# Optimization experiments

Hardware: AMD Instinct MI355X
Metric: run time of the kernel (lower is better)

The kernel has to match this reference:

```python
import jax, jax.numpy as jnp
import numpy as np
import math

SEQLEN, DIM, N_HEADS = 2048, 4096, 32
HEAD_DIM = DIM // N_HEADS
NEG_INF = -1e30  # exp underflows to exactly 0, same effect as -inf without NaN risk


def setup_inputs() -> dict:
    key = jax.random.key(0)
    ks = jax.random.split(key, 7)
    scale = 1.0 / math.sqrt(DIM)
    x = jax.random.normal(ks[0], (SEQLEN, DIM), dtype=jnp.float32)
    weight_q = jax.random.normal(ks[1], (DIM, DIM), dtype=jnp.float32) * scale
    weight_k = jax.random.normal(ks[2], (DIM, DIM), dtype=jnp.float32) * scale
    weight_v = jax.random.normal(ks[3], (DIM, DIM), dtype=jnp.float32) * scale
    weight_o = jax.random.normal(ks[4], (DIM, DIM), dtype=jnp.float32) * scale
    # RoPE frequencies: freqs_cis = exp(i * t * theta_j), standard LLaMA schedule
    inv_freq = 1.0 / (10000.0 ** (np.arange(0, HEAD_DIM, 2, dtype=np.float32) / HEAD_DIM))
    angles = np.arange(SEQLEN, dtype=np.float32)[:, None] * inv_freq[None, :]  # [S, hd/2]
    freqs_cos = jnp.asarray(np.cos(angles), dtype=jnp.float32)
    freqs_sin = jnp.asarray(np.sin(angles), dtype=jnp.float32)
    # additive causal mask [S, S]
    mask = jnp.where(jnp.triu(jnp.ones((SEQLEN, SEQLEN), dtype=bool), k=1), NEG_INF, 0.0).astype(jnp.float32)
    return {"x": x, "weight_q": weight_q, "weight_k": weight_k, "weight_v": weight_v,
            "weight_o": weight_o, "freqs_cos": freqs_cos, "freqs_sin": freqs_sin,
            "mask": mask, "start_pos": 0}


def _apply_rope(t, cos, sin):
    # t: [S, H, hd]; cos/sin: [S, hd/2]
    tr = t.reshape(*t.shape[:-1], -1, 2)           # [S, H, hd/2, 2]
    t_re, t_im = tr[..., 0], tr[..., 1]
    c = cos[:, None, :]
    s = sin[:, None, :]
    out_re = t_re * c - t_im * s
    out_im = t_re * s + t_im * c
    return jnp.stack([out_re, out_im], axis=-1).reshape(t.shape)


def reference(x, weight_q, weight_k, weight_v, weight_o, freqs_cos, freqs_sin, mask, start_pos):
    S, D = x.shape
    hd = freqs_cos.shape[-1] * 2
    H = D // hd
    # the per-head double loop over wq[j][i] is exactly a full [D,D] projection
    xq = (x @ weight_q).reshape(S, H, hd)
    xk = (x @ weight_k).reshape(S, H, hd)
    xv = (x @ weight_v).reshape(S, H, hd)
    xq = _apply_rope(xq, freqs_cos, freqs_sin)
    xk = _apply_rope(xk, freqs_cos, freqs_sin)
    # start_pos == 0 prefill: cache slice == freshly computed keys/values
    scores = jnp.einsum('shd,thd->hst', xq, xk) / jnp.sqrt(jnp.float32(hd))
    scores = scores + mask[None, :, :]
    probs = jax.nn.softmax(scores.astype(jnp.float32), axis=-1).astype(xq.dtype)
    qkv = jnp.einsum('hst,thd->shd', probs, xv).reshape(S, D)
    return qkv @ weight_o
```

## Files before the change

### kernel.cpp

```cpp
#include <hip/hip_runtime.h>
#include <hip/hip_bf16.h>
#include <type_traits>

typedef __hip_bfloat16 bf16;
typedef __attribute__((ext_vector_type(8))) short s8v;
typedef __attribute__((ext_vector_type(4))) short s4v;
typedef __attribute__((ext_vector_type(4))) float f4v;

#define MFMA16(A, B, C) __builtin_amdgcn_mfma_f32_16x16x32_bf16((A), (B), (C), 0, 0, 0)

constexpr int SEQ = 2048;
constexpr int DIM = 4096;
constexpr int NH  = 32;
constexpr int HD  = 128;

__device__ __forceinline__ short f2bs(float f) {
    __hip_bfloat16_raw r = __float2bfloat16(f);
    return (short)r.x;
}

__device__ __forceinline__ void ld_g2l(const bf16* g, bf16* l) {
    __builtin_amdgcn_global_load_lds(
        (const __attribute__((address_space(1))) void*)g,
        (__attribute__((address_space(3))) void*)l, 16, 0, 0);
}

__global__ void convert_bf16(const float* __restrict__ s, bf16* __restrict__ d) {
    int i = blockIdx.x * blockDim.x + threadIdx.x;
    float4 f = ((const float4*)s)[i];
    s4v o;
    o[0] = f2bs(f.x); o[1] = f2bs(f.y); o[2] = f2bs(f.z); o[3] = f2bs(f.w);
    *(s4v*)(d + (size_t)i * 4) = o;
}

__global__ void convt_bf16(const float* __restrict__ src, bf16* __restrict__ dst,
                           int R, int C) {
    __shared__ float t[32][33];
    int c0 = blockIdx.x * 32, r0 = blockIdx.y * 32;
    int tx = threadIdx.x, ty = threadIdx.y;
#pragma unroll
    for (int i = 0; i < 4; i++)
        t[ty + 8 * i][tx] = src[(size_t)(r0 + ty + 8 * i) * C + c0 + tx];
    __syncthreads();
#pragma unroll
    for (int i = 0; i < 4; i++)
        dst[(size_t)(c0 + ty + 8 * i) * R + r0 + tx] = __float2bfloat16(t[tx][ty + 8 * i]);
}

template <typename CT>
__global__ __launch_bounds__(256) void gemm_lds(const bf16* __restrict__ A,
                                                const bf16* __restrict__ Bt,
                                                CT* __restrict__ C,
                                                int M, int N, int K) {
    __shared__ bf16 As[128 * 32];
    __shared__ bf16 Bs[128 * 32];
    const int tid  = threadIdx.x;
    const int lane = tid & 63;
    const int w    = tid >> 6;
    const int m16  = lane & 15;
    const int quad = lane >> 4;
    const int wm   = w >> 1, wn = w & 1;
    const int bm   = blockIdx.y, bn = blockIdx.x;

    const bf16* Ab = A  + (size_t)bm * 128 * K;
    const bf16* Bb = Bt + (size_t)bn * 128 * K;

    const int lrow = lane >> 2;
    const int lcol = (lane & 3) * 8;

    f4v acc[4][4] = {};

    for (int k0 = 0; k0 < K; k0 += 32) {
#pragma unroll
        for (int rep = 0; rep < 2; rep++) {
            int c = w * 2 + rep;
            ld_g2l(Ab + (size_t)(c * 16 + lrow) * K + k0 + lcol, As + c * 512);
            ld_g2l(Bb + (size_t)(c * 16 + lrow) * K + k0 + lcol, Bs + c * 512);
        }
        __syncthreads();

        s8v a[4], b[4];
#pragma unroll
        for (int i = 0; i < 4; i++)
            a[i] = *(s8v*)(As + (wm * 64 + i * 16 + m16) * 32 + quad * 8);
#pragma unroll
        for (int j = 0; j < 4; j++)
            b[j] = *(s8v*)(Bs + (wn * 64 + j * 16 + m16) * 32 + quad * 8);
#pragma unroll
        for (int i = 0; i < 4; i++)
#pragma unroll
            for (int j = 0; j < 4; j++) acc[i][j] = MFMA16(a[i], b[j], acc[i][j]);
        __syncthreads();
    }

#pragma unroll
    for (int i = 0; i < 4; i++)
#pragma unroll
        for (int j = 0; j < 4; j++)
#pragma unroll
            for (int r = 0; r < 4; r++) {
                int row = bm * 128 + wm * 64 + i * 16 + quad * 4 + r;
                int col = bn * 128 + wn * 64 + j * 16 + m16;
                if constexpr (std::is_same<CT, float>::value)
                    C[(size_t)row * N + col] = acc[i][j][r];
                else
                    C[(size_t)row * N + col] = __float2bfloat16(acc[i][j][r]);
            }
}

template <typename AT, typename CT>
__global__ __launch_bounds__(256) void gemm_nat(const AT* __restrict__ A,
                                                const float* __restrict__ B,
                                                CT* __restrict__ C,
                                                int M, int N, int K) {
    __shared__ short As[128][40];
    __shared__ short Bs[128][40];
    const int tid  = threadIdx.x;
    const int lane = tid & 63;
    const int w    = tid >> 6;
    const int m16  = lane & 15;
    const int quad = lane >> 4;
    const int wm   = w >> 1, wn = w & 1;
    const int bm   = blockIdx.y, bn = blockIdx.x;

    const AT* Ab = A + (size_t)bm * 128 * K;

    f4v acc[4][4] = {};
    const int r0 = tid >> 2;
    const int kc = (tid & 3) * 8;

    for (int k0 = 0; k0 < K; k0 += 32) {
        if constexpr (std::is_same<AT, float>::value) {
#pragma unroll
            for (int half = 0; half < 2; half++) {
                const float* src = Ab + (size_t)(r0 + 64 * half) * K + k0 + kc;
                float4 f0 = *(const float4*)(src);
                float4 f1 = *(const float4*)(src + 4);
                s8v t;
                t[0] = f2bs(f0.x); t[1] = f2bs(f0.y); t[2] = f2bs(f0.z); t[3] = f2bs(f0.w);
                t[4] = f2bs(f1.x); t[5] = f2bs(f1.y); t[6] = f2bs(f1.z); t[7] = f2bs(f1.w);
                *(s8v*)&As[r0 + 64 * half][kc] = t;
            }
        } else {
            *(s8v*)&As[r0][kc]      = *(const s8v*)(Ab + (size_t)r0 * K + k0 + kc);
            *(s8v*)&As[r0 + 64][kc] = *(const s8v*)(Ab + (size_t)(r0 + 64) * K + k0 + kc);
        }
#pragma unroll
        for (int v = tid; v < 512; v += 256) {
            int kr = v >> 4;
            int nc = (v & 15) * 8;
            const float* src = B + (size_t)(k0 + kr) * N + bn * 128 + nc;
            float4 f0 = *(const float4*)(src);
            float4 f1 = *(const float4*)(src + 4);
            Bs[nc + 0][kr] = f2bs(f0.x); Bs[nc + 1][kr] = f2bs(f0.y);
            Bs[nc + 2][kr] = f2bs(f0.z); Bs[nc + 3][kr] = f2bs(f0.w);
            Bs[nc + 4][kr] = f2bs(f1.x); Bs[nc + 5][kr] = f2bs(f1.y);
            Bs[nc + 6][kr] = f2bs(f1.z); Bs[nc + 7][kr] = f2bs(f1.w);
        }
        __syncthreads();

        s8v a[4], b[4];
#pragma unroll
        for (int i = 0; i < 4; i++) a[i] = *(s8v*)&As[wm * 64 + i * 16 + m16][quad * 8];
#pragma unroll
        for (int j = 0; j < 4; j++) b[j] = *(s8v*)&Bs[wn * 64 + j * 16 + m16][quad * 8];
#pragma unroll
        for (int i = 0; i < 4; i++)
#pragma unroll
            for (int j = 0; j < 4; j++) acc[i][j] = MFMA16(a[i], b[j], acc[i][j]);
        __syncthreads();
    }

#pragma unroll
    for (int i = 0; i < 4; i++)
#pragma unroll
        for (int j = 0; j < 4; j++)
#pragma unroll
            for (int r = 0; r < 4; r++) {
                int row = bm * 128 + wm * 64 + i * 16 + quad * 4 + r;
                int col = bn * 128 + wn * 64 + j * 16 + m16;
                if constexpr (std::is_same<CT, float>::value)
                    C[(size_t)row * N + col] = acc[i][j][r];
                else
                    C[(size_t)row * N + col] = __float2bfloat16(acc[i][j][r]);
            }
}

__global__ void rope_kernel(bf16* __restrict__ Q, bf16* __restrict__ K,
                            const float* __restrict__ fc, const float* __restrict__ fs) {
    int tid = blockIdx.x * blockDim.x + threadIdx.x;
    int s = tid >> 11;
    int r = tid & 2047;
    int i = r & 63;
    float c  = fc[s * 64 + i];
    float sn = fs[s * 64 + i];
    size_t idx = (size_t)s * DIM + 2 * r;
    float qre = __bfloat162float(Q[idx]), qim = __bfloat162float(Q[idx + 1]);
    Q[idx]     = __float2bfloat16(qre * c - qim * sn);
    Q[idx + 1] = __float2bfloat16(qre * sn + qim * c);
    float kre = __bfloat162float(K[idx]), kim = __bfloat162float(K[idx + 1]);
    K[idx]     = __float2bfloat16(kre * c - kim * sn);
    K[idx + 1] = __float2bfloat16(kre * sn + kim * c);
}

__global__ __launch_bounds__(256) void attn_kernel(const bf16* __restrict__ Q,
                                                   const bf16* __restrict__ K,
                                                   const bf16* __restrict__ V,
                                                   bf16* __restrict__ O) {
    __shared__ short Ks[64][136];
    __shared__ short Vs[128][72];
    __shared__ short Ps[64][72];

    const int qb = (int)gridDim.x - 1 - (int)blockIdx.x;
    const int h  = blockIdx.y;
    const int tid  = threadIdx.x;
    const int w    = tid >> 6;
    const int lane = tid & 63;
    const int m16  = lane & 15;
    const int quad = lane >> 4;
    const float scale = 0.08838834764831845f;

    const int rn  = tid >> 4;
    const int rc  = (tid & 15) * 8;
    const int dcs = (tid & 15) & 7;

    s8v aq[4];
    {
        const bf16* qp = Q + (size_t)(qb * 64 + w * 16 + m16) * DIM + h * HD + quad * 8;
#pragma unroll
        for (int ks = 0; ks < 4; ks++) aq[ks] = *(const s8v*)(qp + ks * 32);
    }

    f4v acc[8] = {};
    float mrow[4] = {-1e30f, -1e30f, -1e30f, -1e30f};
    float lrow[4] = {};

    s8v kreg[4], vreg[4];
    {
        const bf16* kp = K + (size_t)rn * DIM + h * HD + rc;
        const bf16* vp = V + (size_t)rn * DIM + h * HD + rc;
#pragma unroll
        for (int it = 0; it < 4; it++) {
            kreg[it] = *(const s8v*)(kp + (size_t)it * 16 * DIM);
            vreg[it] = *(const s8v*)(vp + (size_t)it * 16 * DIM);
        }
    }

    for (int kt = 0; kt <= qb; kt++) {
#pragma unroll
        for (int it = 0; it < 4; it++)
            *(s8v*)&Ks[it * 16 + rn][rc] = kreg[it];
#pragma unroll
        for (int it = 0; it < 4; it++) {
            int n   = it * 16 + rn;
            int col = (((n >> 3) ^ dcs) << 3) | (n & 7);
#pragma unroll
            for (int e = 0; e < 8; e++) Vs[rc + e][col] = vreg[it][e];
        }
        __syncthreads();

        if (kt < qb) {
            const bf16* kp = K + (size_t)((kt + 1) * 64 + rn) * DIM + h * HD + rc;
            const bf16* vp = V + (size_t)((kt + 1) * 64 + rn) * DIM + h * HD + rc;
#pragma unroll
            for (int it = 0; it < 4; it++) {
                kreg[it] = *(const s8v*)(kp + (size_t)it * 16 * DIM);
                vreg[it] = *(const s8v*)(vp + (size_t)it * 16 * DIM);
            }
        }

        f4v sc[4] = {};
#pragma unroll
        for (int j = 0; j < 4; j++)
#pragma unroll
            for (int ks = 0; ks < 4; ks++) {
                s8v bk = *(s8v*)&Ks[j * 16 + m16][ks * 32 + quad * 8];
                sc[j] = MFMA16(aq[ks], bk, sc[j]);
            }

        const bool diag = (kt == qb);
#pragma unroll
        for (int j = 0; j < 4; j++)
#pragma unroll
            for (int r = 0; r < 4; r++) {
                float sv = sc[j][r] * scale;
                if (diag && (j * 16 + m16) > (w * 16 + quad * 4 + r)) sv = -1e30f;
                sc[j][r] = sv;
            }

#pragma unroll
        for (int r = 0; r < 4; r++) {
            float mx = fmaxf(fmaxf(sc[0][r], sc[1][r]), fmaxf(sc[2][r], sc[3][r]));
#pragma unroll
            for (int off = 1; off < 16; off <<= 1) mx = fmaxf(mx, __shfl_xor(mx, off, 64));
            float mn    = fmaxf(mrow[r], mx);
            float alpha = __expf(mrow[r] - mn);
            mrow[r] = mn;
            float rs = 0.f;
#pragma unroll
            for (int j = 0; j < 4; j++) {
                float p = __expf(sc[j][r] - mn);
                sc[j][r] = p;
                rs += p;
            }
#pragma unroll
            for (int off = 1; off < 16; off <<= 1) rs += __shfl_xor(rs, off, 64);
            lrow[r] = lrow[r] * alpha + rs;
#pragma unroll
            for (int jo = 0; jo < 8; jo++) acc[jo][r] = acc[jo][r] * alpha;
        }

#pragma unroll
        for (int j = 0; j < 4; j++)
#pragma unroll
            for (int r = 0; r < 4; r++)
                Ps[w * 16 + quad * 4 + r][j * 16 + m16] = f2bs(sc[j][r]);
        asm volatile("s_waitcnt lgkmcnt(0)" ::: "memory");
        __builtin_amdgcn_sched_barrier(0);

#pragma unroll
        for (int ks2 = 0; ks2 < 2; ks2++) {
            s8v ap = *(s8v*)&Ps[w * 16 + m16][ks2 * 32 + quad * 8];
#pragma unroll
            for (int jo = 0; jo < 8; jo++) {
                int dv = jo * 16 + m16;
                int cg = (((ks2 * 4 + quad) ^ ((dv >> 3) & 7)) << 3);
                s8v bv = *(s8v*)&Vs[dv][cg];
                acc[jo] = MFMA16(ap, bv, acc[jo]);
            }
        }
        __syncthreads();
    }

#pragma unroll
    for (int jo = 0; jo < 8; jo++)
#pragma unroll
        for (int r = 0; r < 4; r++) {
            float o = acc[jo][r] / fmaxf(lrow[r], 1e-30f);
            int row = qb * 64 + w * 16 + quad * 4 + r;
            int col = h * HD + jo * 16 + m16;
            O[(size_t)row * DIM + col] = __float2bfloat16(o);
        }
}

extern "C" void kernel_launch(void* const* d_in, const int* in_sizes, int n_in,
                              void* d_out, int out_size, void* d_ws, size_t ws_size,
                              hipStream_t stream) {
    const float* x  = (const float*)d_in[0];
    const float* wq = (const float*)d_in[1];
    const float* wk = (const float*)d_in[2];
    const float* wv = (const float*)d_in[3];
    const float* wo = (const float*)d_in[4];
    const float* fc = (const float*)d_in[5];
    const float* fs = (const float*)d_in[6];

    float* out = (float*)d_out;

    const size_t SZ = (size_t)SEQ * DIM;
    const size_t WZ = (size_t)DIM * DIM;
    bf16* Q  = (bf16*)d_ws;
    bf16* Kb = Q + SZ;
    bf16* V  = Kb + SZ;
    bf16* AO = V + SZ;

    dim3 gG(DIM / 128, SEQ / 128);
    const size_t need = (5 * SZ + WZ) * sizeof(bf16);

    if (ws_size >= need) {
        bf16* xb = AO + SZ;
        bf16* wb = xb + SZ;

        dim3 tB(32, 8), tGw(DIM / 32, DIM / 32);

        convert_bf16<<<(int)(SZ / 4 / 256), 256, 0, stream>>>(x, xb);

        convt_bf16<<<tGw, tB, 0, stream>>>(wq, wb, DIM, DIM);
        gemm_lds<bf16><<<gG, 256, 0, stream>>>(xb, wb, Q, SEQ, DIM, DIM);
        convt_bf16<<<tGw, tB, 0, stream>>>(wk, wb, DIM, DIM);
        gemm_lds<bf16><<<gG, 256, 0, stream>>>(xb, wb, Kb, SEQ, DIM, DIM);
        convt_bf16<<<tGw, tB, 0, stream>>>(wv, wb, DIM, DIM);
        gemm_lds<bf16><<<gG, 256, 0, stream>>>(xb, wb, V, SEQ, DIM, DIM);

        rope_kernel<<<(SEQ * (DIM / 2)) / 256, 256, 0, stream>>>(Q, Kb, fc, fs);
        attn_kernel<<<dim3(SEQ / 64, NH), 256, 0, stream>>>(Q, Kb, V, AO);

        convt_bf16<<<tGw, tB, 0, stream>>>(wo, wb, DIM, DIM);
        gemm_lds<float><<<gG, 256, 0, stream>>>(AO, wb, out, SEQ, DIM, DIM);
    } else {
        gemm_nat<float, bf16><<<gG, 256, 0, stream>>>(x, wq, Q,  SEQ, DIM, DIM);
        gemm_nat<float, bf16><<<gG, 256, 0, stream>>>(x, wk, Kb, SEQ, DIM, DIM);
        gemm_nat<float, bf16><<<gG, 256, 0, stream>>>(x, wv, V,  SEQ, DIM, DIM);
        rope_kernel<<<(SEQ * (DIM / 2)) / 256, 256, 0, stream>>>(Q, Kb, fc, fs);
        attn_kernel<<<dim3(SEQ / 64, NH), 256, 0, stream>>>(Q, Kb, V, AO);
        gemm_nat<bf16, float><<<gG, 256, 0, stream>>>(AO, wo, out, SEQ, DIM, DIM);
    }
}
```

Measured before the change: 916.8 us.

## Replace projection GEMM with double-buffered 8-wave 128x256 swizzled-LDS pipelined kernel

Replaces the single-buffered 128x128 K=32 GEMM with a 512-thread 128x256 tile kernel. It uses K=64 double-buffered LDS tiles, XOR-swizzled rows to avoid bank conflicts, and prefetches the next-next stage while computing in quarter-phases with explicit barriers and setprio. This is meant to hide global load latency and raise MFMA utilization in the four projection GEMMs. In exchange it uses much more LDS per block and gives a grid of only 256 blocks, which reduces occupancy and wave-level parallelism.

After: 836.8 us. -8.7%, faster.

```diff
diff --git a/kernel.cpp b/kernel.cpp
--- a/kernel.cpp
+++ b/kernel.cpp
@@ -48,50 +48,118 @@
 }
 
 template <typename CT>
-__global__ __launch_bounds__(256) void gemm_lds(const bf16* __restrict__ A,
-                                                const bf16* __restrict__ Bt,
-                                                CT* __restrict__ C,
-                                                int M, int N, int K) {
-    __shared__ bf16 As[128 * 32];
-    __shared__ bf16 Bs[128 * 32];
+__global__ __launch_bounds__(512, 2) void gemm_8p(const bf16* __restrict__ A,
+                                                  const bf16* __restrict__ Bt,
+                                                  CT* __restrict__ C,
+                                                  int M, int N, int K) {
+    __shared__ bf16 As_[2][128 * 64];
+    __shared__ bf16 Bs_[2][256 * 64];
     const int tid  = threadIdx.x;
     const int lane = tid & 63;
-    const int w    = tid >> 6;
+    const int wv   = tid >> 6;
     const int m16  = lane & 15;
     const int quad = lane >> 4;
-    const int wm   = w >> 1, wn = w & 1;
+    const int wm   = wv >> 2, wn = wv & 3;
     const int bm   = blockIdx.y, bn = blockIdx.x;
 
     const bf16* Ab = A  + (size_t)bm * 128 * K;
-    const bf16* Bb = Bt + (size_t)bn * 128 * K;
-
-    const int lrow = lane >> 2;
-    const int lcol = (lane & 3) * 8;
+    const bf16* Bb = Bt + (size_t)bn * 256 * K;
+
+    const int i0   = wv * 64 + lane;
+    const int row0 = i0 >> 3;
+    const int gc8  = ((i0 & 7) ^ (row0 & 7)) * 8;
+    const int dst0 = (wv * 64) * 8;
+    const int dst1 = (512 + wv * 64) * 8;
+
+    const int aB = (wm * 64 + m16) * 64;
+    const int bB = (wn * 64 + m16) * 64;
+    const int swz = m16 & 7;
+    const int c0k = ((0 + quad) ^ swz) * 8;
+    const int c1k = ((4 + quad) ^ swz) * 8;
+
+    const int NT = K >> 6;
 
     f4v acc[4][4] = {};
-
-    for (int k0 = 0; k0 < K; k0 += 32) {
-#pragma unroll
-        for (int rep = 0; rep < 2; rep++) {
-            int c = w * 2 + rep;
-            ld_g2l(Ab + (size_t)(c * 16 + lrow) * K + k0 + lcol, As + c * 512);
-            ld_g2l(Bb + (size_t)(c * 16 + lrow) * K + k0 + lcol, Bs + c * 512);
-        }
-        __syncthreads();
-
-        s8v a[4], b[4];
-#pragma unroll
-        for (int i = 0; i < 4; i++)
-            a[i] = *(s8v*)(As + (wm * 64 + i * 16 + m16) * 32 + quad * 8);
-#pragma unroll
-        for (int j = 0; j < 4; j++)
-            b[j] = *(s8v*)(Bs + (wn * 64 + j * 16 + m16) * 32 + quad * 8);
-#pragma unroll
-        for (int i = 0; i < 4; i++)
-#pragma unroll
-            for (int j = 0; j < 4; j++) acc[i][j] = MFMA16(a[i], b[j], acc[i][j]);
-        __syncthreads();
-    }
+    s8v aR[4][2], bR[4][2];
+
+#define STAGEU(gb, lb) do { \
+        ld_g2l((gb) + (size_t)row0 * K + gc8, (lb) + dst0); \
+        ld_g2l((gb) + (size_t)(row0 + 64) * K + gc8, (lb) + dst1); } while (0)
+#define LDA_(i, ks) aR[i][ks] = *(const s8v*)(Ac + aB + (i) * 1024 + ((ks) ? c1k : c0k))
+#define LDB_(j, ks) bR[j][ks] = *(const s8v*)(Bc + bB + (j) * 1024 + ((ks) ? c1k : c0k))
+#define MMQ(i, j) do { acc[i][j] = MFMA16(aR[i][0], bR[j][0], acc[i][j]); \
+                       acc[i][j] = MFMA16(aR[i][1], bR[j][1], acc[i][j]); } while (0)
+#define BARX()  __builtin_amdgcn_s_barrier()
+#define LGKM0() do { asm volatile("s_waitcnt lgkmcnt(0)" ::: "memory"); \
+                     __builtin_amdgcn_sched_barrier(0); } while (0)
+
+    STAGEU(Ab, As_[0]);
+    STAGEU(Bb, Bs_[0]);
+    STAGEU(Bb + (size_t)128 * K, Bs_[0] + 128 * 64);
+    if (NT > 1) {
+        STAGEU(Bb + 64, Bs_[1]);
+        STAGEU(Bb + (size_t)128 * K + 64, Bs_[1] + 128 * 64);
+        STAGEU(Ab + 64, As_[1]);
+        asm volatile("s_waitcnt vmcnt(6)" ::: "memory");
+    } else {
+        asm volatile("s_waitcnt vmcnt(0)" ::: "memory");
+    }
+    __builtin_amdgcn_sched_barrier(0);
+    BARX();
+
+    for (int t = 0; t < NT; ++t) {
+        const int cur = t & 1;
+        const bf16* Ac = As_[cur];
+        const bf16* Bc = Bs_[cur];
+        const bool more = (t + 2 < NT);
+        const int k2 = (t + 2) << 6;
+
+        LDA_(0, 0); LDA_(0, 1); LDA_(1, 0); LDA_(1, 1);
+        LDB_(0, 0); LDB_(0, 1); LDB_(1, 0); LDB_(1, 1);
+        BARX(); LGKM0();
+        __builtin_amdgcn_s_setprio(1);
+        MMQ(0, 0); MMQ(0, 1); MMQ(1, 0); MMQ(1, 1);
+        __builtin_amdgcn_s_setprio(0);
+        BARX();
+
+        LDB_(2, 0); LDB_(2, 1); LDB_(3, 0); LDB_(3, 1);
+        BARX(); LGKM0();
+        __builtin_amdgcn_s_setprio(1);
+        MMQ(0, 2); MMQ(0, 3); MMQ(1, 2); MMQ(1, 3);
+        __builtin_amdgcn_s_setprio(0);
+        BARX();
+
+        LDA_(2, 0); LDA_(2, 1); LDA_(3, 0); LDA_(3, 1);
+        if (more) {
+            STAGEU(Bb + k2, Bs_[cur]);
+            STAGEU(Bb + (size_t)128 * K + k2, Bs_[cur] + 128 * 64);
+        }
+        BARX(); LGKM0();
+        __builtin_amdgcn_s_setprio(1);
+        MMQ(2, 0); MMQ(2, 1); MMQ(3, 0); MMQ(3, 1);
+        __builtin_amdgcn_s_setprio(0);
+        BARX();
+
+        if (more) {
+            STAGEU(Ab + k2, As_[cur]);
+            asm volatile("s_waitcnt vmcnt(6)" ::: "memory");
+        } else {
+            asm volatile("s_waitcnt vmcnt(0)" ::: "memory");
+        }
+        __builtin_amdgcn_sched_barrier(0);
+        BARX();
+        __builtin_amdgcn_s_setprio(1);
+        MMQ(2, 2); MMQ(2, 3); MMQ(3, 2); MMQ(3, 3);
+        __builtin_amdgcn_s_setprio(0);
+        BARX();
+    }
+
+#undef STAGEU
+#undef LDA_
+#undef LDB_
+#undef MMQ
+#undef BARX
+#undef LGKM0
 
 #pragma unroll
     for (int i = 0; i < 4; i++)
@@ -100,7 +168,7 @@
 #pragma unroll
             for (int r = 0; r < 4; r++) {
                 int row = bm * 128 + wm * 64 + i * 16 + quad * 4 + r;
-                int col = bn * 128 + wn * 64 + j * 16 + m16;
+                int col = bn * 256 + wn * 64 + j * 16 + m16;
                 if constexpr (std::is_same<CT, float>::value)
                     C[(size_t)row * N + col] = acc[i][j][r];
                 else
@@ -363,7 +431,6 @@
     bf16* V  = Kb + SZ;
     bf16* AO = V + SZ;
 
-    dim3 gG(DIM / 128, SEQ / 128);
     const size_t need = (5 * SZ + WZ) * sizeof(bf16);
 
     if (ws_size >= need) {
@@ -371,27 +438,29 @@
         bf16* wb = xb + SZ;
 
         dim3 tB(32, 8), tGw(DIM / 32, DIM / 32);
+        dim3 gG8(DIM / 256, SEQ / 128);
 
         convert_bf16<<<(int)(SZ / 4 / 256), 256, 0, stream>>>(x, xb);
 
         convt_bf16<<<tGw, tB, 0, stream>>>(wq, wb, DIM, DIM);
-        gemm_lds<bf16><<<gG, 256, 0, stream>>>(xb, wb, Q, SEQ, DIM, DIM);
+        gemm_8p<bf16><<<gG8, 512, 0, stream>>>(xb, wb, Q, SEQ, DIM, DIM);
         convt_bf16<<<tGw, tB, 0, stream>>>(wk, wb, DIM, DIM);
-        gemm_lds<bf16><<<gG, 256, 0, stream>>>(xb, wb, Kb, SEQ, DIM, DIM);
+        gemm_8p<bf16><<<gG8, 512, 0, stream>>>(xb, wb, Kb, SEQ, DIM, DIM);
         convt_bf16<<<tGw, tB, 0, stream>>>(wv, wb, DIM, DIM);
-        gemm_lds<bf16><<<gG, 256, 0, stream>>>(xb, wb, V, SEQ, DIM, DIM);
+        gemm_8p<bf16><<<gG8, 512, 0, stream>>>(xb, wb, V, SEQ, DIM, DIM);
 
         rope_kernel<<<(SEQ * (DIM / 2)) / 256, 256, 0, stream>>>(Q, Kb, fc, fs);
         attn_kernel<<<dim3(SEQ / 64, NH), 256, 0, stream>>>(Q, Kb, V, AO);
 
         convt_bf16<<<tGw, tB, 0, stream>>>(wo, wb, DIM, DIM);
-        gemm_lds<float><<<gG, 256, 0, stream>>>(AO, wb, out, SEQ, DIM, DIM);
+        gemm_8p<float><<<gG8, 512, 0, stream>>>(AO, wb, out, SEQ, DIM, DIM);
     } else {
-        gemm_nat<float, bf16><<<gG, 256, 0, stream>>>(x, wq, Q,  SEQ, DIM, DIM);
-        gemm_nat<float, bf16><<<gG, 256, 0, stream>>>(x, wk, Kb, SEQ, DIM, DIM);
-        gemm_nat<float, bf16><<<gG, 256, 0, stream>>>(x, wv, V,  SEQ, DIM, DIM);
+        dim3 gGn(DIM / 128, SEQ / 128);
+        gemm_nat<float, bf16><<<gGn, 256, 0, stream>>>(x, wq, Q,  SEQ, DIM, DIM);
+        gemm_nat<float, bf16><<<gGn, 256, 0, stream>>>(x, wk, Kb, SEQ, DIM, DIM);
+        gemm_nat<float, bf16><<<gGn, 256, 0, stream>>>(x, wv, V,  SEQ, DIM, DIM);
         rope_kernel<<<(SEQ * (DIM / 2)) / 256, 256, 0, stream>>>(Q, Kb, fc, fs);
         attn_kernel<<<dim3(SEQ / 64, NH), 256, 0, stream>>>(Q, Kb, V, AO);
-        gemm_nat<bf16, float><<<gG, 256, 0, stream>>>(AO, wo, out, SEQ, DIM, DIM);
-    }
-}
+        gemm_nat<bf16, float><<<gGn, 256, 0, stream>>>(AO, wo, out, SEQ, DIM, DIM);
+    }
+}
```
